# Kernel tuning notes

Hardware: AMD Instinct MI355X
Metric: run time of the kernel (lower is better)

## Reference

```python
import jax, jax.numpy as jnp
import numpy as np

N = 100000   # nodes
E = 3200000  # directed edges (avg degree 32)
T = 2048     # total flattened orders across all moves
M = 256      # number of moves (segments)


def _gat(x, src, dst, Wl, bl, Wr, br, att, b):
    # GATv2Conv (heads=1, eval mode -> attention dropout off), with self loops
    xl = x @ Wl.T + bl              # [N,10]
    xr = x @ Wr.T + br              # [N,10]
    sl = jnp.arange(N)
    s = jnp.concatenate([src, sl])
    d = jnp.concatenate([dst, sl])
    e = jax.nn.leaky_relu(xl[s] + xr[d], 0.2) @ att    # [E+N]
    emax = jax.ops.segment_max(e, d, num_segments=N)
    ex = jnp.exp(e - emax[d])
    den = jax.ops.segment_sum(ex, d, num_segments=N)
    return jax.ops.segment_sum((ex / den[d])[:, None] * xl[s], d, num_segments=N) + b


def setup_inputs() -> dict:
    key = jax.random.key(0)
    ks = iter(jax.random.split(key, 64))
    rn = lambda shape, s=0.1: jax.random.normal(next(ks), shape, jnp.float32) * s
    inp = {}
    inp['x1'] = rn((N, 15), 1.0)
    inp['x2'] = rn((1, 4), 1.0)
    src = jax.random.randint(next(ks), (E,), 0, N, jnp.int32)
    off = jax.random.randint(next(ks), (E,), 1, N, jnp.int32)
    inp['edge_src'] = src
    inp['edge_dst'] = ((src + off) % N).astype(jnp.int32)
    inp['move_type'] = jax.random.randint(next(ks), (T,), 0, 2, jnp.int32)
    inp['m_src'] = jax.random.randint(next(ks), (T,), 0, N, jnp.int32)
    inp['m_dst'] = jax.random.randint(next(ks), (T,), 0, N, jnp.int32)
    inp['m_target'] = jax.random.randint(next(ks), (T,), 0, N, jnp.int32)
    inp['m_armies'] = jax.random.uniform(next(ks), (T,), jnp.float32) * 10.0
    inp['move_id'] = (jnp.arange(T, dtype=jnp.int32) // (T // M))  # sorted, all segments non-empty
    # GATv2 layer params (in dims 15, 25, 25 -> out 10)
    for i, din in [(1, 15), (2, 25), (3, 25)]:
        inp[f'Wl{i}'] = rn((10, din)); inp[f'bl{i}'] = rn((10,))
        inp[f'Wr{i}'] = rn((10, din)); inp[f'br{i}'] = rn((10,))
        inp[f'att{i}'] = rn((10,));   inp[f'bias{i}'] = rn((10,))
    inp['lin_W'] = rn((15, 29)); inp['lin_b'] = rn((15,))
    inp['lin2_W'] = rn((1, 15)); inp['lin2_b'] = rn((1,))
    inp['aaa_W'] = rn((20, 48)); inp['aaa_b'] = rn((20,))
    inp['ccc_W'] = rn((20, 23)); inp['ccc_b'] = rn((20,))
    inp['attl_W'] = rn((1, 20)); inp['attl_b'] = rn((1,))
    inp['pi_W'] = rn((1, 20));   inp['pi_b'] = rn((1,))
    return inp


def reference(x1, x2, edge_src, edge_dst, move_type, m_src, m_dst, m_target, m_armies, move_id,
              Wl1, bl1, Wr1, br1, att1, bias1,
              Wl2, bl2, Wr2, br2, att2, bias2,
              Wl3, bl3, Wr3, br3, att3, bias3,
              lin_W, lin_b, lin2_W, lin2_b, aaa_W, aaa_b, ccc_W, ccc_b,
              attl_W, attl_b, pi_W, pi_b):
    h = jax.nn.relu(_gat(x1, edge_src, edge_dst, Wl1, bl1, Wr1, br1, att1, bias1))
    h = jax.nn.relu(_gat(jnp.concatenate([h, x1], 1), edge_src, edge_dst, Wl2, bl2, Wr2, br2, att2, bias2))
    x = jax.nn.relu(_gat(jnp.concatenate([h, x1], 1), edge_src, edge_dst, Wl3, bl3, Wr3, br3, att3, bias3))

    # per-order features (both branches computed, selected by move_type)
    extra = (0.6 * m_armies - 0.7 * (x1[m_dst, 3] + x1[m_dst, 4]))[:, None]
    feat_a = jnp.concatenate([x[m_src], x[m_dst], x1[m_src, 3:], x1[m_dst, 1:], m_armies[:, None], extra], axis=1)  # [T,48]
    a_out = jax.nn.relu(feat_a @ aaa_W.T + aaa_b)
    feat_d = jnp.concatenate([x[m_target], x1[m_target, 3:], m_armies[:, None]], axis=1)  # [T,23]
    d_out = jax.nn.relu(feat_d @ ccc_W.T + ccc_b)
    hm = jnp.where((move_type == 0)[:, None], a_out, d_out)  # [T,20]

    al = (hm @ attl_W.T + attl_b)[:, 0]   # [T]
    pi = (hm @ pi_W.T + pi_b)[:, 0]       # [T]
    amax = jax.ops.segment_max(al, move_id, num_segments=M)
    ex = jnp.exp(al - amax[move_id])
    den = jax.ops.segment_sum(ex, move_id, num_segments=M)
    p = jax.ops.segment_sum(ex / den[move_id] * pi, move_id, num_segments=M)  # [M]
    logp = jax.nn.log_softmax(p)

    x2t = jnp.tile(x2, (N, 1))
    v = jax.nn.relu(jnp.concatenate([x, x1, x2t], 1) @ lin_W.T + lin_b)
    V = jnp.tanh(jnp.mean(v @ lin2_W.T + lin2_b))
    return (V, logp)
```

## Files before the change

kernel.cpp:

```cpp
#include <hip/hip_runtime.h>
#include <cmath>

#define NN 100000
#define NE 3200000
#define TT 2048
#define MM 256
#define STR 16
#define HSTR 16
#define BSZ 64
#define NB 1563
#define EPB 16384
#define NBLK 196
#define SCAP 3072
#define PCAP 4096
#define CMAX 12
#define SRTP_CAP 5500000

__device__ __forceinline__ void atomicMaxF(float* addr, float v) {
    if (v >= 0.f) atomicMax((int*)addr, __float_as_int(v));
    else          atomicMin((unsigned int*)addr, __float_as_uint(v));
}

__device__ __forceinline__ unsigned short f2bf(float x) {
    unsigned u = __float_as_uint(x);
    u += 0x7FFFu + ((u >> 16) & 1u);
    return (unsigned short)(u >> 16);
}

__device__ __forceinline__ void unpack10(uint4 q, unsigned q2, float* a) {
    a[0] = __uint_as_float(q.x << 16);
    a[1] = __uint_as_float(q.x & 0xFFFF0000u);
    a[2] = __uint_as_float(q.y << 16);
    a[3] = __uint_as_float(q.y & 0xFFFF0000u);
    a[4] = __uint_as_float(q.z << 16);
    a[5] = __uint_as_float(q.z & 0xFFFF0000u);
    a[6] = __uint_as_float(q.w << 16);
    a[7] = __uint_as_float(q.w & 0xFFFF0000u);
    a[8] = __uint_as_float(q2 << 16);
    a[9] = __uint_as_float(q2 & 0xFFFF0000u);
}

__global__ __launch_bounds__(1024) void init_kernel(int* bcounts, int* pcounts, float* amax,
                                                    float* den_m, float* num_m, float* Vsum) {
    int i = blockIdx.x * 1024 + threadIdx.x;
    if (i < NB) { bcounts[i] = 0; pcounts[i] = 0; }
    if (i < MM) { amax[i] = -INFINITY; den_m[i] = 0.f; num_m[i] = 0.f; }
    if (i == 0) Vsum[0] = 0.f;
}

__global__ __launch_bounds__(256) void hist_kernel(const int* __restrict__ dst,
                                                   int* __restrict__ bcounts,
                                                   int* __restrict__ pcounts) {
    __shared__ int h[NB];
    int tid = threadIdx.x;
    for (int i = tid; i < NB; i += 256) h[i] = 0;
    __syncthreads();
    int base = blockIdx.x * EPB;
    int end = base + EPB; if (end > NE) end = NE;
    for (int i = base + tid * 4; i < end; i += 1024) {
        int4 d4 = *(const int4*)(dst + i);
        atomicAdd(&h[d4.x >> 6], 1);
        atomicAdd(&h[d4.y >> 6], 1);
        atomicAdd(&h[d4.z >> 6], 1);
        atomicAdd(&h[d4.w >> 6], 1);
    }
    __syncthreads();
    for (int i = tid; i < NB; i += 256) {
        int n = h[i];
        if (n) {
            atomicAdd(&bcounts[i], n);
            atomicAdd(&pcounts[i], (n + 15) & ~15);
        }
    }
}

__global__ __launch_bounds__(1024) void scan_kernel(const int* __restrict__ bcounts,
                                                    const int* __restrict__ pcounts,
                                                    int* __restrict__ bstart,
                                                    int* __restrict__ pbstart,
                                                    int* __restrict__ pcursor) {
    __shared__ int ssum[1024];
    __shared__ int psum[1024];
    int tid = threadIdx.x;
    const int per = (NB + 1023) / 1024;
    int base = tid * per;
    int s = 0, p = 0;
    for (int i = 0; i < per; i++) {
        int idx = base + i;
        if (idx < NB) { s += bcounts[idx]; p += pcounts[idx]; }
    }
    ssum[tid] = s; psum[tid] = p;
    __syncthreads();
    for (int off = 1; off < 1024; off <<= 1) {
        int v = (tid >= off) ? ssum[tid - off] : 0;
        int w = (tid >= off) ? psum[tid - off] : 0;
        __syncthreads();
        ssum[tid] += v; psum[tid] += w;
        __syncthreads();
    }
    int run = ssum[tid] - s;
    int prun = psum[tid] - p;
    for (int i = 0; i < per; i++) {
        int idx = base + i;
        if (idx < NB) {
            bstart[idx] = run;              run += bcounts[idx];
            pbstart[idx] = prun;
            pcursor[idx] = prun;            prun += pcounts[idx];
        }
    }
    if (tid == 0) { bstart[NB] = NE; pbstart[NB] = psum[1023]; }
}

__global__ __launch_bounds__(1024) void scatter_kernel(const int* __restrict__ src,
                                                       const int* __restrict__ dst,
                                                       int* __restrict__ pcursor,
                                                       int* __restrict__ srtp) {
    __shared__ int ent[EPB];
    __shared__ int cnt[NB];
    __shared__ int cur[NB];
    __shared__ int gbase[NB];
    __shared__ int psc[1024];
    int tid = threadIdx.x;
    for (int i = tid; i < NB; i += 1024) cnt[i] = 0;
    __syncthreads();
    int base = blockIdx.x * EPB;
    int end = base + EPB; if (end > NE) end = NE;
    for (int i = base + tid * 4; i < end; i += 4096) {
        int4 d4 = *(const int4*)(dst + i);
        atomicAdd(&cnt[d4.x >> 6], 1);
        atomicAdd(&cnt[d4.y >> 6], 1);
        atomicAdd(&cnt[d4.z >> 6], 1);
        atomicAdd(&cnt[d4.w >> 6], 1);
    }
    __syncthreads();
    const int PT = (NB + 1023) / 1024;
    int t0 = tid * PT;
    int s = 0;
    #pragma unroll
    for (int j = 0; j < PT; j++) { int idx = t0 + j; if (idx < NB) s += cnt[idx]; }
    psc[tid] = s;
    __syncthreads();
    for (int off = 1; off < 1024; off <<= 1) {
        int v = (tid >= off) ? psc[tid - off] : 0;
        __syncthreads();
        psc[tid] += v;
        __syncthreads();
    }
    int run = psc[tid] - s;
    #pragma unroll
    for (int j = 0; j < PT; j++) {
        int idx = t0 + j;
        if (idx < NB) { cur[idx] = run; run += cnt[idx]; }
    }
    for (int b = tid; b < NB; b += 1024) {
        int n = cnt[b];
        gbase[b] = n ? atomicAdd(&pcursor[b], (n + 15) & ~15) : 0;
    }
    __syncthreads();
    for (int i = base + tid * 4; i < end; i += 4096) {
        int4 d4 = *(const int4*)(dst + i);
        int4 s4 = *(const int4*)(src + i);
        int d, b, off;
        d = d4.x; b = d >> 6; off = atomicAdd(&cur[b], 1); ent[off] = ((d & 63) << 17) | s4.x;
        d = d4.y; b = d >> 6; off = atomicAdd(&cur[b], 1); ent[off] = ((d & 63) << 17) | s4.y;
        d = d4.z; b = d >> 6; off = atomicAdd(&cur[b], 1); ent[off] = ((d & 63) << 17) | s4.z;
        d = d4.w; b = d >> 6; off = atomicAdd(&cur[b], 1); ent[off] = ((d & 63) << 17) | s4.w;
    }
    __syncthreads();
    for (int b = tid; b < NB; b += 1024) {
        int n = cnt[b];
        if (!n) continue;
        int lb = cur[b] - n;
        int gb = gbase[b];
        int p16 = (n + 15) & ~15;
        for (int k = 0; k < p16; k += 4) {
            int4 v;
            v.x = (k + 0 < n) ? ent[lb + k + 0] : -1;
            v.y = (k + 1 < n) ? ent[lb + k + 1] : -1;
            v.z = (k + 2 < n) ? ent[lb + k + 2] : -1;
            v.w = (k + 3 < n) ? ent[lb + k + 3] : -1;
            *(int4*)(srtp + gb + k) = v;
        }
    }
}

__global__ __launch_bounds__(512) void sort2_kernel(const int* __restrict__ srtp,
                                                    const int* __restrict__ pbstart,
                                                    const int* __restrict__ bstart,
                                                    int* __restrict__ srt) {
    __shared__ int ent[PCAP];
    __shared__ int ent2[SCAP];
    __shared__ int cnts[BSZ];
    __shared__ int curs[BSZ];
    int b = blockIdx.x, tid = threadIdx.x;
    int p0 = pbstart[b], p1 = pbstart[b + 1];
    int pcnt = p1 - p0;
    if (pcnt > PCAP) pcnt = PCAP;
    if (tid < BSZ) cnts[tid] = 0;
    __syncthreads();
    for (int i = tid; i < pcnt; i += 512) {
        int p = srtp[p0 + i];
        ent[i] = p;
        if (p >= 0) atomicAdd(&cnts[p >> 17], 1);
    }
    __syncthreads();
    if (tid == 0) {
        int run = 0;
        for (int k = 0; k < BSZ; k++) { curs[k] = run; run += cnts[k]; }
    }
    __syncthreads();
    for (int i = tid; i < pcnt; i += 512) {
        int p = ent[i];
        if (p >= 0) {
            int pos = atomicAdd(&curs[p >> 17], 1);
            ent2[pos] = p;
        }
    }
    __syncthreads();
    int i0 = bstart[b];
    int cnt = bstart[b + 1] - i0;
    for (int i = tid; i < cnt; i += 512) srt[i0 + i] = ent2[i];
}

__global__ __launch_bounds__(256) void prep_kernel(
    const float* __restrict__ hprev,
    const float* __restrict__ x1,
    const float* __restrict__ Wl, const float* __restrict__ bl,
    const float* __restrict__ Wr, const float* __restrict__ br,
    unsigned short* __restrict__ xlh,
    unsigned short* __restrict__ xrh,
    int din)
{
    __shared__ float sWl[250], sWr[250], sbl[10], sbr[10];
    int tid = threadIdx.x;
    int nw = 10 * din;
    for (int i = tid; i < nw; i += blockDim.x) { sWl[i] = Wl[i]; sWr[i] = Wr[i]; }
    if (tid < 10) { sbl[tid] = bl[tid]; sbr[tid] = br[tid]; }
    __syncthreads();
    int n = blockIdx.x * blockDim.x + tid;
    if (n >= NN) return;

    float in[25];
    if (din == 15) {
        #pragma unroll
        for (int k = 0; k < 15; k++) in[k] = x1[n * 15 + k];
    } else {
        #pragma unroll
        for (int k = 0; k < 10; k++) in[k] = hprev[n * STR + k];
        #pragma unroll
        for (int k = 0; k < 15; k++) in[10 + k] = x1[n * 15 + k];
    }

    float slv[10], srv[10];
    #pragma unroll
    for (int j = 0; j < 10; j++) {
        float sl = sbl[j], sr = sbr[j];
        for (int k = 0; k < din; k++) {
            sl += in[k] * sWl[j * din + k];
            sr += in[k] * sWr[j * din + k];
        }
        slv[j] = sl; srv[j] = sr;
    }
    unsigned* lp = (unsigned*)(xlh + n * HSTR);
    unsigned* rp = (unsigned*)(xrh + n * HSTR);
    #pragma unroll
    for (int j = 0; j < 5; j++) {
        lp[j] = (unsigned)f2bf(slv[2 * j]) | ((unsigned)f2bf(slv[2 * j + 1]) << 16);
        rp[j] = (unsigned)f2bf(srv[2 * j]) | ((unsigned)f2bf(srv[2 * j + 1]) << 16);
    }
}

__global__ __launch_bounds__(256, 4) void gather_kernel(
    const int* __restrict__ srt, const int* __restrict__ bstart,
    const unsigned short* __restrict__ xlh, const unsigned short* __restrict__ xrh,
    const float* __restrict__ att, const float* __restrict__ bias,
    float* __restrict__ hout)
{
    __shared__ float accs[BSZ * 11];
    __shared__ float xrs[BSZ * 11];
    __shared__ float sat[10];
    int b = blockIdx.x, tid = threadIdx.x;
    if (tid < 10) sat[tid] = att[tid];
    __syncthreads();

    int n0 = b * BSZ;
    if (tid < BSZ) {
        int n = n0 + tid;
        if (n < NN) {
            const unsigned short* lr = xlh + n * HSTR;
            const unsigned short* rr = xrh + n * HSTR;
            uint4 ql = *(const uint4*)lr;  unsigned ql2 = *(const unsigned*)(lr + 8);
            uint4 qr = *(const uint4*)rr;  unsigned qr2 = *(const unsigned*)(rr + 8);
            float a[10], r[10];
            unpack10(ql, ql2, a);
            unpack10(qr, qr2, r);
            #pragma unroll
            for (int k = 0; k < 10; k++) xrs[tid * 11 + k] = r[k];
            float e = 0.f;
            #pragma unroll
            for (int k = 0; k < 10; k++) {
                float t = a[k] + r[k];
                t = t > 0.f ? t : 0.2f * t;
                e += sat[k] * t;
            }
            float ex = __expf(e);
            #pragma unroll
            for (int k = 0; k < 10; k++) accs[tid * 11 + k] = ex * a[k];
            accs[tid * 11 + 10] = ex;
        } else {
            #pragma unroll
            for (int k = 0; k < 11; k++) { accs[tid * 11 + k] = 0.f; xrs[tid * 11 + k] = 0.f; }
        }
    }
    __syncthreads();

    int i0 = bstart[b], i1 = bstart[b + 1];
    int cnt = i1 - i0;
    int C = (cnt + 255) >> 8;
    int a0 = i0 + tid * C;
    int a1 = a0 + C; if (a1 > i1) a1 = i1;
    int len = a1 - a0; if (len < 0) len = 0;
    if (len > 0) {
        int ps[CMAX];
        #pragma unroll
        for (int i = 0; i < CMAX; i++) ps[i] = (i < len) ? srt[a0 + i] : -1;

        const unsigned short* row0 = xlh + (ps[0] & 0x1FFFF) * HSTR;
        uint4 q = *(const uint4*)row0;
        unsigned q2 = *(const unsigned*)(row0 + 8);
        int cur = ps[0] >> 17;
        float racc[10];
        #pragma unroll
        for (int k = 0; k < 10; k++) racc[k] = 0.f;
        float rden = 0.f;
        #pragma unroll
        for (int i = 0; i < CMAX; i++) {
            if (i >= len) break;
            uint4 qn = q; unsigned q2n = q2;
            if (i + 1 < len) {
                const unsigned short* rn = xlh + (ps[i + 1] & 0x1FFFF) * HSTR;
                qn = *(const uint4*)rn;
                q2n = *(const unsigned*)(rn + 8);
            }
            int ld = ps[i] >> 17;
            if (ld != cur) {
                float* ac = accs + cur * 11;
                #pragma unroll
                for (int k = 0; k < 10; k++) atomicAdd(ac + k, racc[k]);
                atomicAdd(ac + 10, rden);
                #pragma unroll
                for (int k = 0; k < 10; k++) racc[k] = 0.f;
                rden = 0.f;
                cur = ld;
            }
            float a[10];
            unpack10(q, q2, a);
            const float* r = xrs + ld * 11;
            float e = 0.f;
            #pragma unroll
            for (int k = 0; k < 10; k++) {
                float t = a[k] + r[k];
                t = t > 0.f ? t : 0.2f * t;
                e += sat[k] * t;
            }
            float ex = __expf(e);
            rden += ex;
            #pragma unroll
            for (int k = 0; k < 10; k++) racc[k] += ex * a[k];
            q = qn; q2 = q2n;
        }
        float* ac = accs + cur * 11;
        #pragma unroll
        for (int k = 0; k < 10; k++) atomicAdd(ac + k, racc[k]);
        atomicAdd(ac + 10, rden);
    }
    __syncthreads();

    if (tid < BSZ) {
        int n = n0 + tid;
        if (n < NN) {
            float inv = 1.f / accs[tid * 11 + 10];
            #pragma unroll
            for (int k = 0; k < 10; k++) {
                float v = accs[tid * 11 + k] * inv + bias[k];
                hout[n * STR + k] = v > 0.f ? v : 0.f;
            }
        }
    }
}

__global__ __launch_bounds__(256) void value_kernel(
    const float* __restrict__ x, const float* __restrict__ x1, const float* __restrict__ x2,
    const float* __restrict__ lin_W, const float* __restrict__ lin_b,
    const float* __restrict__ lin2_W, const float* __restrict__ lin2_b,
    float* __restrict__ Vsum)
{
    __shared__ float sW[15 * 29], sb[15], sW2[15];
    __shared__ float red[256];
    int tid = threadIdx.x;
    for (int i = tid; i < 15 * 29; i += 256) sW[i] = lin_W[i];
    if (tid < 15) { sb[tid] = lin_b[tid]; sW2[tid] = lin2_W[tid]; }
    __syncthreads();
    int n = blockIdx.x * 256 + tid;
    float local = 0.f;
    if (n < NN) {
        float in[29];
        #pragma unroll
        for (int k = 0; k < 10; k++) in[k] = x[n * STR + k];
        #pragma unroll
        for (int k = 0; k < 15; k++) in[10 + k] = x1[n * 15 + k];
        #pragma unroll
        for (int k = 0; k < 4; k++) in[25 + k] = x2[k];
        float sc = lin2_b[0];
        #pragma unroll
        for (int j = 0; j < 15; j++) {
            float s = sb[j];
            for (int k = 0; k < 29; k++) s += in[k] * sW[j * 29 + k];
            sc += (s > 0.f ? s : 0.f) * sW2[j];
        }
        local = sc;
    }
    red[tid] = local;
    __syncthreads();
    for (int off = 128; off > 0; off >>= 1) {
        if (tid < off) red[tid] += red[tid + off];
        __syncthreads();
    }
    if (tid == 0) atomicAdd(Vsum, red[0]);
}

__global__ __launch_bounds__(256) void orders_kernel(
    const float* __restrict__ x, const float* __restrict__ x1,
    const int* __restrict__ move_type, const int* __restrict__ m_src,
    const int* __restrict__ m_dst, const int* __restrict__ m_target,
    const float* __restrict__ m_armies, const int* __restrict__ move_id,
    const float* __restrict__ aaa_W, const float* __restrict__ aaa_b,
    const float* __restrict__ ccc_W, const float* __restrict__ ccc_b,
    const float* __restrict__ attl_W, const float* __restrict__ attl_b,
    const float* __restrict__ pi_W, const float* __restrict__ pi_b,
    float* __restrict__ al_out, float* __restrict__ pi_out, float* __restrict__ amax)
{
    __shared__ float sA[20 * 48], sC[20 * 23], sAb[20], sCb[20];
    int tid = threadIdx.x;
    for (int i = tid; i < 20 * 48; i += 256) sA[i] = aaa_W[i];
    for (int i = tid; i < 20 * 23; i += 256) sC[i] = ccc_W[i];
    if (tid < 20) { sAb[tid] = aaa_b[tid]; sCb[tid] = ccc_b[tid]; }
    __syncthreads();
    int t = blockIdx.x * 256 + tid;
    if (t >= TT) return;

    float armies = m_armies[t];
    float hm[20];
    if (move_type[t] == 0) {
        int sn = m_src[t], dn = m_dst[t];
        float f[48];
        #pragma unroll
        for (int k = 0; k < 10; k++) f[k] = x[sn * STR + k];
        #pragma unroll
        for (int k = 0; k < 10; k++) f[10 + k] = x[dn * STR + k];
        #pragma unroll
        for (int k = 0; k < 12; k++) f[20 + k] = x1[sn * 15 + 3 + k];
        #pragma unroll
        for (int k = 0; k < 14; k++) f[32 + k] = x1[dn * 15 + 1 + k];
        f[46] = armies;
        f[47] = 0.6f * armies - 0.7f * (x1[dn * 15 + 3] + x1[dn * 15 + 4]);
        #pragma unroll
        for (int j = 0; j < 20; j++) {
            float s = sAb[j];
            for (int k = 0; k < 48; k++) s += f[k] * sA[j * 48 + k];
            hm[j] = s > 0.f ? s : 0.f;
        }
    } else {
        int tg = m_target[t];
        float f[23];
        #pragma unroll
        for (int k = 0; k < 10; k++) f[k] = x[tg * STR + k];
        #pragma unroll
        for (int k = 0; k < 12; k++) f[10 + k] = x1[tg * 15 + 3 + k];
        f[22] = armies;
        #pragma unroll
        for (int j = 0; j < 20; j++) {
            float s = sCb[j];
            for (int k = 0; k < 23; k++) s += f[k] * sC[j * 23 + k];
            hm[j] = s > 0.f ? s : 0.f;
        }
    }
    float a = attl_b[0], p = pi_b[0];
    #pragma unroll
    for (int j = 0; j < 20; j++) { a += hm[j] * attl_W[j]; p += hm[j] * pi_W[j]; }
    al_out[t] = a;
    pi_out[t] = p;
    atomicMaxF(&amax[move_id[t]], a);
}

__global__ __launch_bounds__(256) void orders2_kernel(
    const float* __restrict__ al, const float* __restrict__ piv,
    const int* __restrict__ move_id, const float* __restrict__ amax,
    float* __restrict__ den_m, float* __restrict__ num_m)
{
    int t = blockIdx.x * 256 + threadIdx.x;
    if (t >= TT) return;
    int m = move_id[t];
    float ex = __expf(al[t] - amax[m]);
    atomicAdd(den_m + m, ex);
    atomicAdd(num_m + m, ex * piv[t]);
}

__global__ __launch_bounds__(256) void final_kernel(
    const float* __restrict__ num_m, const float* __restrict__ den_m,
    const float* __restrict__ Vsum, float* __restrict__ out)
{
    __shared__ float sh[256];
    __shared__ float s_max, s_sum;
    int m = threadIdx.x;
    float p = num_m[m] / den_m[m];
    sh[m] = p;
    __syncthreads();
    for (int off = 128; off > 0; off >>= 1) {
        if (m < off) sh[m] = fmaxf(sh[m], sh[m + off]);
        __syncthreads();
    }
    if (m == 0) s_max = sh[0];
    __syncthreads();
    float e = __expf(p - s_max);
    sh[m] = e;
    __syncthreads();
    for (int off = 128; off > 0; off >>= 1) {
        if (m < off) sh[m] += sh[m + off];
        __syncthreads();
    }
    if (m == 0) s_sum = sh[0];
    __syncthreads();
    out[1 + m] = p - s_max - logf(s_sum);
    if (m == 0) out[0] = tanhf(Vsum[0] / (float)NN);
}

extern "C" void kernel_launch(void* const* d_in, const int* in_sizes, int n_in,
                              void* d_out, int out_size, void* d_ws, size_t ws_size,
                              hipStream_t stream) {
    const float* x1        = (const float*)d_in[0];
    const float* x2        = (const float*)d_in[1];
    const int*   esrc      = (const int*)d_in[2];
    const int*   edst      = (const int*)d_in[3];
    const int*   move_type = (const int*)d_in[4];
    const int*   m_src     = (const int*)d_in[5];
    const int*   m_dst     = (const int*)d_in[6];
    const int*   m_target  = (const int*)d_in[7];
    const float* m_armies  = (const float*)d_in[8];
    const int*   move_id   = (const int*)d_in[9];
    const float* W[3][6];
    for (int l = 0; l < 3; l++)
        for (int j = 0; j < 6; j++)
            W[l][j] = (const float*)d_in[10 + l * 6 + j];
    const float* lin_W  = (const float*)d_in[28];
    const float* lin_b  = (const float*)d_in[29];
    const float* lin2_W = (const float*)d_in[30];
    const float* lin2_b = (const float*)d_in[31];
    const float* aaa_W  = (const float*)d_in[32];
    const float* aaa_b  = (const float*)d_in[33];
    const float* ccc_W  = (const float*)d_in[34];
    const float* ccc_b  = (const float*)d_in[35];
    const float* attl_W = (const float*)d_in[36];
    const float* attl_b = (const float*)d_in[37];
    const float* pi_W   = (const float*)d_in[38];
    const float* pi_b   = (const float*)d_in[39];

    float* ws = (float*)d_ws;
    float* hA    = ws; ws += NN * STR;
    float* al    = ws; ws += TT;
    float* piv   = ws; ws += TT;
    float* amax  = ws; ws += MM;
    float* den_m = ws; ws += MM;
    float* num_m = ws; ws += MM;
    float* Vsum  = ws; ws += 1;
    unsigned short* xlh = (unsigned short*)ws; ws += NN * HSTR / 2;
    unsigned short* xrh = (unsigned short*)ws; ws += NN * HSTR / 2;
    int* iws = (int*)ws;
    int* bcounts = iws; iws += NB;
    int* pcounts = iws; iws += NB;
    int* bstart  = iws; iws += NB + 1;
    int* pbstart = iws; iws += NB + 1;
    int* pcursor = iws; iws += NB;
    int* srt     = iws; iws += NE;
    int* srtp    = iws; iws += SRTP_CAP;

    dim3 blk(256);
    dim3 gN((NN + 255) / 256);
    dim3 gT(TT / 256);

    init_kernel<<<dim3(2), dim3(1024), 0, stream>>>(bcounts, pcounts, amax, den_m, num_m, Vsum);
    hist_kernel<<<dim3(NBLK), blk, 0, stream>>>(edst, bcounts, pcounts);
    scan_kernel<<<dim3(1), dim3(1024), 0, stream>>>(bcounts, pcounts, bstart, pbstart, pcursor);
    scatter_kernel<<<dim3(NBLK), dim3(1024), 0, stream>>>(esrc, edst, pcursor, srtp);
    sort2_kernel<<<dim3(NB), dim3(512), 0, stream>>>(srtp, pbstart, bstart, srt);

    prep_kernel<<<gN, blk, 0, stream>>>(nullptr, x1, W[0][0], W[0][1], W[0][2], W[0][3], xlh, xrh, 15);
    gather_kernel<<<dim3(NB), blk, 0, stream>>>(srt, bstart, xlh, xrh, W[0][4], W[0][5], hA);

    prep_kernel<<<gN, blk, 0, stream>>>(hA, x1, W[1][0], W[1][1], W[1][2], W[1][3], xlh, xrh, 25);
    gather_kernel<<<dim3(NB), blk, 0, stream>>>(srt, bstart, xlh, xrh, W[1][4], W[1][5], hA);

    prep_kernel<<<gN, blk, 0, stream>>>(hA, x1, W[2][0], W[2][1], W[2][2], W[2][3], xlh, xrh, 25);
    gather_kernel<<<dim3(NB), blk, 0, stream>>>(srt, bstart, xlh, xrh, W[2][4], W[2][5], hA);

    value_kernel<<<gN, blk, 0, stream>>>(hA, x1, x2, lin_W, lin_b, lin2_W, lin2_b, Vsum);
    orders_kernel<<<gT, blk, 0, stream>>>(hA, x1, move_type, m_src, m_dst, m_target,
                                          m_armies, move_id, aaa_W, aaa_b, ccc_W, ccc_b,
                                          attl_W, attl_b, pi_W, pi_b, al, piv, amax);
    orders2_kernel<<<gT, blk, 0, stream>>>(al, piv, move_id, amax, den_m, num_m);
    final_kernel<<<dim3(1), blk, 0, stream>>>(num_m, den_m, Vsum, (float*)d_out);
}
```

Measured before the change: 437.8 us.

## Drop histogram/scan with fixed-capacity buckets and fuse GAT layers with next projection

Removes the histogram and prefix-scan passes by giving each destination bucket a fixed PCAP-sized slot. Bucket cursors are initialised inside the first projection kernel, and sort2 now sorts in place and records per-bucket counts. Each gather kernel now computes the next layer's bf16 projections, using double-buffered xl/xr arrays, and the last gather also computes the value head. The orders reduction is folded into the final kernel with shared-memory atomics. This cuts about eight launches and the intermediate hA round trips, at the cost of a larger padded workspace and silent truncation if any bucket exceeds PCAP.

```diff
diff --git a/kernel.cpp b/kernel.cpp
--- a/kernel.cpp
+++ b/kernel.cpp
@@ -14,7 +14,6 @@
 #define SCAP 3072
 #define PCAP 4096
 #define CMAX 12
-#define SRTP_CAP 5500000
 
 __device__ __forceinline__ void atomicMaxF(float* addr, float v) {
     if (v >= 0.f) atomicMax((int*)addr, __float_as_int(v));
@@ -40,75 +39,45 @@
     a[9] = __uint_as_float(q2 & 0xFFFF0000u);
 }
 
-__global__ __launch_bounds__(1024) void init_kernel(int* bcounts, int* pcounts, float* amax,
-                                                    float* den_m, float* num_m, float* Vsum) {
-    int i = blockIdx.x * 1024 + threadIdx.x;
-    if (i < NB) { bcounts[i] = 0; pcounts[i] = 0; }
-    if (i < MM) { amax[i] = -INFINITY; den_m[i] = 0.f; num_m[i] = 0.f; }
-    if (i == 0) Vsum[0] = 0.f;
-}
-
-__global__ __launch_bounds__(256) void hist_kernel(const int* __restrict__ dst,
-                                                   int* __restrict__ bcounts,
-                                                   int* __restrict__ pcounts) {
-    __shared__ int h[NB];
+__global__ __launch_bounds__(256) void init_prep1_kernel(
+    const float* __restrict__ x1,
+    const float* __restrict__ Wl, const float* __restrict__ bl,
+    const float* __restrict__ Wr, const float* __restrict__ br,
+    unsigned short* __restrict__ xlh, unsigned short* __restrict__ xrh,
+    int* __restrict__ pcursor, float* __restrict__ amax, float* __restrict__ Vsum)
+{
+    __shared__ float sWl[150], sWr[150], sbl[10], sbr[10];
     int tid = threadIdx.x;
-    for (int i = tid; i < NB; i += 256) h[i] = 0;
-    __syncthreads();
-    int base = blockIdx.x * EPB;
-    int end = base + EPB; if (end > NE) end = NE;
-    for (int i = base + tid * 4; i < end; i += 1024) {
-        int4 d4 = *(const int4*)(dst + i);
-        atomicAdd(&h[d4.x >> 6], 1);
-        atomicAdd(&h[d4.y >> 6], 1);
-        atomicAdd(&h[d4.z >> 6], 1);
-        atomicAdd(&h[d4.w >> 6], 1);
-    }
-    __syncthreads();
-    for (int i = tid; i < NB; i += 256) {
-        int n = h[i];
-        if (n) {
-            atomicAdd(&bcounts[i], n);
-            atomicAdd(&pcounts[i], (n + 15) & ~15);
-        }
-    }
-}
-
-__global__ __launch_bounds__(1024) void scan_kernel(const int* __restrict__ bcounts,
-                                                    const int* __restrict__ pcounts,
-                                                    int* __restrict__ bstart,
-                                                    int* __restrict__ pbstart,
-                                                    int* __restrict__ pcursor) {
-    __shared__ int ssum[1024];
-    __shared__ int psum[1024];
-    int tid = threadIdx.x;
-    const int per = (NB + 1023) / 1024;
-    int base = tid * per;
-    int s = 0, p = 0;
-    for (int i = 0; i < per; i++) {
-        int idx = base + i;
-        if (idx < NB) { s += bcounts[idx]; p += pcounts[idx]; }
-    }
-    ssum[tid] = s; psum[tid] = p;
-    __syncthreads();
-    for (int off = 1; off < 1024; off <<= 1) {
-        int v = (tid >= off) ? ssum[tid - off] : 0;
-        int w = (tid >= off) ? psum[tid - off] : 0;
-        __syncthreads();
-        ssum[tid] += v; psum[tid] += w;
-        __syncthreads();
-    }
-    int run = ssum[tid] - s;
-    int prun = psum[tid] - p;
-    for (int i = 0; i < per; i++) {
-        int idx = base + i;
-        if (idx < NB) {
-            bstart[idx] = run;              run += bcounts[idx];
-            pbstart[idx] = prun;
-            pcursor[idx] = prun;            prun += pcounts[idx];
-        }
-    }
-    if (tid == 0) { bstart[NB] = NE; pbstart[NB] = psum[1023]; }
+    for (int i = tid; i < 150; i += 256) { sWl[i] = Wl[i]; sWr[i] = Wr[i]; }
+    if (tid < 10) { sbl[tid] = bl[tid]; sbr[tid] = br[tid]; }
+    __syncthreads();
+    int gid = blockIdx.x * 256 + tid;
+    if (gid < NB) pcursor[gid] = gid * PCAP;
+    if (gid < MM) amax[gid] = -INFINITY;
+    if (gid == 0) Vsum[0] = 0.f;
+    int n = gid;
+    if (n >= NN) return;
+
+    float in[15];
+    #pragma unroll
+    for (int k = 0; k < 15; k++) in[k] = x1[n * 15 + k];
+
+    unsigned* lp = (unsigned*)(xlh + n * HSTR);
+    unsigned* rp = (unsigned*)(xrh + n * HSTR);
+    #pragma unroll
+    for (int jp = 0; jp < 5; jp++) {
+        float sl0 = sbl[2 * jp], sr0 = sbr[2 * jp];
+        float sl1 = sbl[2 * jp + 1], sr1 = sbr[2 * jp + 1];
+        for (int k = 0; k < 15; k++) {
+            float v = in[k];
+            sl0 += v * sWl[(2 * jp) * 15 + k];
+            sr0 += v * sWr[(2 * jp) * 15 + k];
+            sl1 += v * sWl[(2 * jp + 1) * 15 + k];
+            sr1 += v * sWr[(2 * jp + 1) * 15 + k];
+        }
+        lp[jp] = (unsigned)f2bf(sl0) | ((unsigned)f2bf(sl1) << 16);
+        rp[jp] = (unsigned)f2bf(sr0) | ((unsigned)f2bf(sr1) << 16);
+    }
 }
 
 __global__ __launch_bounds__(1024) void scatter_kernel(const int* __restrict__ src,
@@ -184,17 +153,16 @@
     }
 }
 
-__global__ __launch_bounds__(512) void sort2_kernel(const int* __restrict__ srtp,
-                                                    const int* __restrict__ pbstart,
-                                                    const int* __restrict__ bstart,
-                                                    int* __restrict__ srt) {
+__global__ __launch_bounds__(512) void sort2_kernel(int* __restrict__ srtp,
+                                                    const int* __restrict__ pcursor,
+                                                    int* __restrict__ bcounts) {
     __shared__ int ent[PCAP];
     __shared__ int ent2[SCAP];
     __shared__ int cnts[BSZ];
     __shared__ int curs[BSZ];
     int b = blockIdx.x, tid = threadIdx.x;
-    int p0 = pbstart[b], p1 = pbstart[b + 1];
-    int pcnt = p1 - p0;
+    int p0 = b * PCAP;
+    int pcnt = pcursor[b] - p0;
     if (pcnt > PCAP) pcnt = PCAP;
     if (tid < BSZ) cnts[tid] = 0;
     __syncthreads();
@@ -217,70 +185,27 @@
         }
     }
     __syncthreads();
-    int i0 = bstart[b];
-    int cnt = bstart[b + 1] - i0;
-    for (int i = tid; i < cnt; i += 512) srt[i0 + i] = ent2[i];
-}
-
-__global__ __launch_bounds__(256) void prep_kernel(
-    const float* __restrict__ hprev,
-    const float* __restrict__ x1,
-    const float* __restrict__ Wl, const float* __restrict__ bl,
-    const float* __restrict__ Wr, const float* __restrict__ br,
-    unsigned short* __restrict__ xlh,
-    unsigned short* __restrict__ xrh,
-    int din)
-{
-    __shared__ float sWl[250], sWr[250], sbl[10], sbr[10];
-    int tid = threadIdx.x;
-    int nw = 10 * din;
-    for (int i = tid; i < nw; i += blockDim.x) { sWl[i] = Wl[i]; sWr[i] = Wr[i]; }
-    if (tid < 10) { sbl[tid] = bl[tid]; sbr[tid] = br[tid]; }
-    __syncthreads();
-    int n = blockIdx.x * blockDim.x + tid;
-    if (n >= NN) return;
-
-    float in[25];
-    if (din == 15) {
-        #pragma unroll
-        for (int k = 0; k < 15; k++) in[k] = x1[n * 15 + k];
-    } else {
-        #pragma unroll
-        for (int k = 0; k < 10; k++) in[k] = hprev[n * STR + k];
-        #pragma unroll
-        for (int k = 0; k < 15; k++) in[10 + k] = x1[n * 15 + k];
-    }
-
-    float slv[10], srv[10];
-    #pragma unroll
-    for (int j = 0; j < 10; j++) {
-        float sl = sbl[j], sr = sbr[j];
-        for (int k = 0; k < din; k++) {
-            sl += in[k] * sWl[j * din + k];
-            sr += in[k] * sWr[j * din + k];
-        }
-        slv[j] = sl; srv[j] = sr;
-    }
-    unsigned* lp = (unsigned*)(xlh + n * HSTR);
-    unsigned* rp = (unsigned*)(xrh + n * HSTR);
-    #pragma unroll
-    for (int j = 0; j < 5; j++) {
-        lp[j] = (unsigned)f2bf(slv[2 * j]) | ((unsigned)f2bf(slv[2 * j + 1]) << 16);
-        rp[j] = (unsigned)f2bf(srv[2 * j]) | ((unsigned)f2bf(srv[2 * j + 1]) << 16);
-    }
-}
-
-__global__ __launch_bounds__(256, 4) void gather_kernel(
-    const int* __restrict__ srt, const int* __restrict__ bstart,
+    int cnt = curs[BSZ - 1];
+    for (int i = tid; i < cnt; i += 512) srtp[p0 + i] = ent2[i];
+    if (tid == 0) bcounts[b] = cnt;
+}
+
+__global__ __launch_bounds__(256, 4) void gather_mid_kernel(
+    const int* __restrict__ srtp, const int* __restrict__ bcounts,
     const unsigned short* __restrict__ xlh, const unsigned short* __restrict__ xrh,
     const float* __restrict__ att, const float* __restrict__ bias,
-    float* __restrict__ hout)
+    const float* __restrict__ x1,
+    const float* __restrict__ Wl2, const float* __restrict__ bl2,
+    const float* __restrict__ Wr2, const float* __restrict__ br2,
+    unsigned short* __restrict__ xlh_out, unsigned short* __restrict__ xrh_out)
 {
     __shared__ float accs[BSZ * 11];
     __shared__ float xrs[BSZ * 11];
     __shared__ float sat[10];
+    __shared__ float sWl2[250], sWr2[250], sbl2[10], sbr2[10];
     int b = blockIdx.x, tid = threadIdx.x;
-    if (tid < 10) sat[tid] = att[tid];
+    if (tid < 10) { sat[tid] = att[tid]; sbl2[tid] = bl2[tid]; sbr2[tid] = br2[tid]; }
+    for (int i = tid; i < 250; i += 256) { sWl2[i] = Wl2[i]; sWr2[i] = Wr2[i]; }
     __syncthreads();
 
     int n0 = b * BSZ;
@@ -314,16 +239,16 @@
     }
     __syncthreads();
 
-    int i0 = bstart[b], i1 = bstart[b + 1];
-    int cnt = i1 - i0;
+    int i0 = b * PCAP;
+    int cnt = bcounts[b];
     int C = (cnt + 255) >> 8;
     int a0 = i0 + tid * C;
-    int a1 = a0 + C; if (a1 > i1) a1 = i1;
+    int a1 = a0 + C; if (a1 > i0 + cnt) a1 = i0 + cnt;
     int len = a1 - a0; if (len < 0) len = 0;
     if (len > 0) {
         int ps[CMAX];
         #pragma unroll
-        for (int i = 0; i < CMAX; i++) ps[i] = (i < len) ? srt[a0 + i] : -1;
+        for (int i = 0; i < CMAX; i++) ps[i] = (i < len) ? srtp[a0 + i] : -1;
 
         const unsigned short* row0 = xlh + (ps[0] & 0x1FFFF) * HSTR;
         uint4 q = *(const uint4*)row0;
@@ -380,53 +305,181 @@
         int n = n0 + tid;
         if (n < NN) {
             float inv = 1.f / accs[tid * 11 + 10];
+            float in[25];
             #pragma unroll
             for (int k = 0; k < 10; k++) {
                 float v = accs[tid * 11 + k] * inv + bias[k];
-                hout[n * STR + k] = v > 0.f ? v : 0.f;
-            }
-        }
-    }
-}
-
-__global__ __launch_bounds__(256) void value_kernel(
-    const float* __restrict__ x, const float* __restrict__ x1, const float* __restrict__ x2,
+                in[k] = v > 0.f ? v : 0.f;
+            }
+            #pragma unroll
+            for (int k = 0; k < 15; k++) in[10 + k] = x1[n * 15 + k];
+            unsigned* lp = (unsigned*)(xlh_out + n * HSTR);
+            unsigned* rp = (unsigned*)(xrh_out + n * HSTR);
+            #pragma unroll
+            for (int jp = 0; jp < 5; jp++) {
+                float sl0 = sbl2[2 * jp], sr0 = sbr2[2 * jp];
+                float sl1 = sbl2[2 * jp + 1], sr1 = sbr2[2 * jp + 1];
+                for (int k = 0; k < 25; k++) {
+                    float v = in[k];
+                    sl0 += v * sWl2[(2 * jp) * 25 + k];
+                    sr0 += v * sWr2[(2 * jp) * 25 + k];
+                    sl1 += v * sWl2[(2 * jp + 1) * 25 + k];
+                    sr1 += v * sWr2[(2 * jp + 1) * 25 + k];
+                }
+                lp[jp] = (unsigned)f2bf(sl0) | ((unsigned)f2bf(sl1) << 16);
+                rp[jp] = (unsigned)f2bf(sr0) | ((unsigned)f2bf(sr1) << 16);
+            }
+        }
+    }
+}
+
+__global__ __launch_bounds__(256, 4) void gather_last_kernel(
+    const int* __restrict__ srtp, const int* __restrict__ bcounts,
+    const unsigned short* __restrict__ xlh, const unsigned short* __restrict__ xrh,
+    const float* __restrict__ att, const float* __restrict__ bias,
+    const float* __restrict__ x1, const float* __restrict__ x2,
     const float* __restrict__ lin_W, const float* __restrict__ lin_b,
     const float* __restrict__ lin2_W, const float* __restrict__ lin2_b,
-    float* __restrict__ Vsum)
+    float* __restrict__ hout, float* __restrict__ Vsum)
 {
-    __shared__ float sW[15 * 29], sb[15], sW2[15];
-    __shared__ float red[256];
-    int tid = threadIdx.x;
-    for (int i = tid; i < 15 * 29; i += 256) sW[i] = lin_W[i];
-    if (tid < 15) { sb[tid] = lin_b[tid]; sW2[tid] = lin2_W[tid]; }
-    __syncthreads();
-    int n = blockIdx.x * 256 + tid;
+    __shared__ float accs[BSZ * 11];
+    __shared__ float xrs[BSZ * 11];
+    __shared__ float sat[10];
+    __shared__ float sLW[15 * 29], sLb[15], sW2[15], sx2[4];
+    __shared__ float slin2b;
+    int b = blockIdx.x, tid = threadIdx.x;
+    if (tid < 10) sat[tid] = att[tid];
+    for (int i = tid; i < 15 * 29; i += 256) sLW[i] = lin_W[i];
+    if (tid < 15) { sLb[tid] = lin_b[tid]; sW2[tid] = lin2_W[tid]; }
+    if (tid < 4) sx2[tid] = x2[tid];
+    if (tid == 0) slin2b = lin2_b[0];
+    __syncthreads();
+
+    int n0 = b * BSZ;
+    if (tid < BSZ) {
+        int n = n0 + tid;
+        if (n < NN) {
+            const unsigned short* lr = xlh + n * HSTR;
+            const unsigned short* rr = xrh + n * HSTR;
+            uint4 ql = *(const uint4*)lr;  unsigned ql2 = *(const unsigned*)(lr + 8);
+            uint4 qr = *(const uint4*)rr;  unsigned qr2 = *(const unsigned*)(rr + 8);
+            float a[10], r[10];
+            unpack10(ql, ql2, a);
+            unpack10(qr, qr2, r);
+            #pragma unroll
+            for (int k = 0; k < 10; k++) xrs[tid * 11 + k] = r[k];
+            float e = 0.f;
+            #pragma unroll
+            for (int k = 0; k < 10; k++) {
+                float t = a[k] + r[k];
+                t = t > 0.f ? t : 0.2f * t;
+                e += sat[k] * t;
+            }
+            float ex = __expf(e);
+            #pragma unroll
+            for (int k = 0; k < 10; k++) accs[tid * 11 + k] = ex * a[k];
+            accs[tid * 11 + 10] = ex;
+        } else {
+            #pragma unroll
+            for (int k = 0; k < 11; k++) { accs[tid * 11 + k] = 0.f; xrs[tid * 11 + k] = 0.f; }
+        }
+    }
+    __syncthreads();
+
+    int i0 = b * PCAP;
+    int cnt = bcounts[b];
+    int C = (cnt + 255) >> 8;
+    int a0 = i0 + tid * C;
+    int a1 = a0 + C; if (a1 > i0 + cnt) a1 = i0 + cnt;
+    int len = a1 - a0; if (len < 0) len = 0;
+    if (len > 0) {
+        int ps[CMAX];
+        #pragma unroll
+        for (int i = 0; i < CMAX; i++) ps[i] = (i < len) ? srtp[a0 + i] : -1;
+
+        const unsigned short* row0 = xlh + (ps[0] & 0x1FFFF) * HSTR;
+        uint4 q = *(const uint4*)row0;
+        unsigned q2 = *(const unsigned*)(row0 + 8);
+        int cur = ps[0] >> 17;
+        float racc[10];
+        #pragma unroll
+        for (int k = 0; k < 10; k++) racc[k] = 0.f;
+        float rden = 0.f;
+        #pragma unroll
+        for (int i = 0; i < CMAX; i++) {
+            if (i >= len) break;
+            uint4 qn = q; unsigned q2n = q2;
+            if (i + 1 < len) {
+                const unsigned short* rn = xlh + (ps[i + 1] & 0x1FFFF) * HSTR;
+                qn = *(const uint4*)rn;
+                q2n = *(const unsigned*)(rn + 8);
+            }
+            int ld = ps[i] >> 17;
+            if (ld != cur) {
+                float* ac = accs + cur * 11;
+                #pragma unroll
+                for (int k = 0; k < 10; k++) atomicAdd(ac + k, racc[k]);
+                atomicAdd(ac + 10, rden);
+                #pragma unroll
+                for (int k = 0; k < 10; k++) racc[k] = 0.f;
+                rden = 0.f;
+                cur = ld;
+            }
+            float a[10];
+            unpack10(q, q2, a);
+            const float* r = xrs + ld * 11;
+            float e = 0.f;
+            #pragma unroll
+            for (int k = 0; k < 10; k++) {
+                float t = a[k] + r[k];
+                t = t > 0.f ? t : 0.2f * t;
+                e += sat[k] * t;
+            }
+            float ex = __expf(e);
+            rden += ex;
+            #pragma unroll
+            for (int k = 0; k < 10; k++) racc[k] += ex * a[k];
+            q = qn; q2 = q2n;
+        }
+        float* ac = accs + cur * 11;
+        #pragma unroll
+        for (int k = 0; k < 10; k++) atomicAdd(ac + k, racc[k]);
+        atomicAdd(ac + 10, rden);
+    }
+    __syncthreads();
+
     float local = 0.f;
-    if (n < NN) {
-        float in[29];
-        #pragma unroll
-        for (int k = 0; k < 10; k++) in[k] = x[n * STR + k];
-        #pragma unroll
-        for (int k = 0; k < 15; k++) in[10 + k] = x1[n * 15 + k];
-        #pragma unroll
-        for (int k = 0; k < 4; k++) in[25 + k] = x2[k];
-        float sc = lin2_b[0];
-        #pragma unroll
-        for (int j = 0; j < 15; j++) {
-            float s = sb[j];
-            for (int k = 0; k < 29; k++) s += in[k] * sW[j * 29 + k];
-            sc += (s > 0.f ? s : 0.f) * sW2[j];
-        }
-        local = sc;
-    }
-    red[tid] = local;
-    __syncthreads();
-    for (int off = 128; off > 0; off >>= 1) {
-        if (tid < off) red[tid] += red[tid + off];
-        __syncthreads();
-    }
-    if (tid == 0) atomicAdd(Vsum, red[0]);
+    if (tid < BSZ) {
+        int n = n0 + tid;
+        if (n < NN) {
+            float inv = 1.f / accs[tid * 11 + 10];
+            float in[29];
+            #pragma unroll
+            for (int k = 0; k < 10; k++) {
+                float v = accs[tid * 11 + k] * inv + bias[k];
+                v = v > 0.f ? v : 0.f;
+                hout[n * STR + k] = v;
+                in[k] = v;
+            }
+            #pragma unroll
+            for (int k = 0; k < 15; k++) in[10 + k] = x1[n * 15 + k];
+            #pragma unroll
+            for (int k = 0; k < 4; k++) in[25 + k] = sx2[k];
+            float sc = slin2b;
+            #pragma unroll
+            for (int j = 0; j < 15; j++) {
+                float s = sLb[j];
+                for (int k = 0; k < 29; k++) s += in[k] * sLW[j * 29 + k];
+                sc += (s > 0.f ? s : 0.f) * sW2[j];
+            }
+            local = sc;
+        }
+    }
+    if (tid < 64) {
+        #pragma unroll
+        for (int off = 32; off > 0; off >>= 1) local += __shfl_down(local, off, 64);
+        if (tid == 0) atomicAdd(Vsum, local);
+    }
 }
 
 __global__ __launch_bounds__(256) void orders_kernel(
@@ -493,27 +546,25 @@
     atomicMaxF(&amax[move_id[t]], a);
 }
 
-__global__ __launch_bounds__(256) void orders2_kernel(
+__global__ __launch_bounds__(256) void final2_kernel(
     const float* __restrict__ al, const float* __restrict__ piv,
     const int* __restrict__ move_id, const float* __restrict__ amax,
-    float* __restrict__ den_m, float* __restrict__ num_m)
-{
-    int t = blockIdx.x * 256 + threadIdx.x;
-    if (t >= TT) return;
-    int m = move_id[t];
-    float ex = __expf(al[t] - amax[m]);
-    atomicAdd(den_m + m, ex);
-    atomicAdd(num_m + m, ex * piv[t]);
-}
-
-__global__ __launch_bounds__(256) void final_kernel(
-    const float* __restrict__ num_m, const float* __restrict__ den_m,
     const float* __restrict__ Vsum, float* __restrict__ out)
 {
+    __shared__ float den_s[MM], num_s[MM];
     __shared__ float sh[256];
     __shared__ float s_max, s_sum;
     int m = threadIdx.x;
-    float p = num_m[m] / den_m[m];
+    den_s[m] = 0.f; num_s[m] = 0.f;
+    __syncthreads();
+    for (int t = m; t < TT; t += 256) {
+        int mid = move_id[t];
+        float ex = __expf(al[t] - amax[mid]);
+        atomicAdd(&den_s[mid], ex);
+        atomicAdd(&num_s[mid], ex * piv[t]);
+    }
+    __syncthreads();
+    float p = num_s[m] / den_s[m];
     sh[m] = p;
     __syncthreads();
     for (int off = 128; off > 0; off >>= 1) {
@@ -570,43 +621,40 @@
     float* al    = ws; ws += TT;
     float* piv   = ws; ws += TT;
     float* amax  = ws; ws += MM;
-    float* den_m = ws; ws += MM;
-    float* num_m = ws; ws += MM;
     float* Vsum  = ws; ws += 1;
-    unsigned short* xlh = (unsigned short*)ws; ws += NN * HSTR / 2;
-    unsigned short* xrh = (unsigned short*)ws; ws += NN * HSTR / 2;
+    unsigned short* xlhA = (unsigned short*)ws; ws += NN * HSTR / 2;
+    unsigned short* xrhA = (unsigned short*)ws; ws += NN * HSTR / 2;
+    unsigned short* xlhB = (unsigned short*)ws; ws += NN * HSTR / 2;
+    unsigned short* xrhB = (unsigned short*)ws; ws += NN * HSTR / 2;
     int* iws = (int*)ws;
+    int* pcursor = iws; iws += NB;
     int* bcounts = iws; iws += NB;
-    int* pcounts = iws; iws += NB;
-    int* bstart  = iws; iws += NB + 1;
-    int* pbstart = iws; iws += NB + 1;
-    int* pcursor = iws; iws += NB;
-    int* srt     = iws; iws += NE;
-    int* srtp    = iws; iws += SRTP_CAP;
+    int* srtp    = iws; iws += NB * PCAP;
 
     dim3 blk(256);
     dim3 gN((NN + 255) / 256);
     dim3 gT(TT / 256);
 
-    init_kernel<<<dim3(2), dim3(1024), 0, stream>>>(bcounts, pcounts, amax, den_m, num_m, Vsum);
-    hist_kernel<<<dim3(NBLK), blk, 0, stream>>>(edst, bcounts, pcounts);
-    scan_kernel<<<dim3(1), dim3(1024), 0, stream>>>(bcounts, pcounts, bstart, pbstart, pcursor);
+    init_prep1_kernel<<<gN, blk, 0, stream>>>(x1, W[0][0], W[0][1], W[0][2], W[0][3],
+                                              xlhA, xrhA, pcursor, amax, Vsum);
     scatter_kernel<<<dim3(NBLK), dim3(1024), 0, stream>>>(esrc, edst, pcursor, srtp);
-    sort2_kernel<<<dim3(NB), dim3(512), 0, stream>>>(srtp, pbstart, bstart, srt);
-
-    prep_kernel<<<gN, blk, 0, stream>>>(nullptr, x1, W[0][0], W[0][1], W[0][2], W[0][3], xlh, xrh, 15);
-    gather_kernel<<<dim3(NB), blk, 0, stream>>>(srt, bstart, xlh, xrh, W[0][4], W[0][5], hA);
-
-    prep_kernel<<<gN, blk, 0, stream>>>(hA, x1, W[1][0], W[1][1], W[1][2], W[1][3], xlh, xrh, 25);
-    gather_kernel<<<dim3(NB), blk, 0, stream>>>(srt, bstart, xlh, xrh, W[1][4], W[1][5], hA);
-
-    prep_kernel<<<gN, blk, 0, stream>>>(hA, x1, W[2][0], W[2][1], W[2][2], W[2][3], xlh, xrh, 25);
-    gather_kernel<<<dim3(NB), blk, 0, stream>>>(srt, bstart, xlh, xrh, W[2][4], W[2][5], hA);
-
-    value_kernel<<<gN, blk, 0, stream>>>(hA, x1, x2, lin_W, lin_b, lin2_W, lin2_b, Vsum);
+    sort2_kernel<<<dim3(NB), dim3(512), 0, stream>>>(srtp, pcursor, bcounts);
+
+    gather_mid_kernel<<<dim3(NB), blk, 0, stream>>>(srtp, bcounts, xlhA, xrhA,
+                                                    W[0][4], W[0][5], x1,
+                                                    W[1][0], W[1][1], W[1][2], W[1][3],
+                                                    xlhB, xrhB);
+    gather_mid_kernel<<<dim3(NB), blk, 0, stream>>>(srtp, bcounts, xlhB, xrhB,
+                                                    W[1][4], W[1][5], x1,
+                                                    W[2][0], W[2][1], W[2][2], W[2][3],
+                                                    xlhA, xrhA);
+    gather_last_kernel<<<dim3(NB), blk, 0, stream>>>(srtp, bcounts, xlhA, xrhA,
+                                                     W[2][4], W[2][5], x1, x2,
+                                                     lin_W, lin_b, lin2_W, lin2_b,
+                                                     hA, Vsum);
+
     orders_kernel<<<gT, blk, 0, stream>>>(hA, x1, move_type, m_src, m_dst, m_target,
                                           m_armies, move_id, aaa_W, aaa_b, ccc_W, ccc_b,
                                           attl_W, attl_b, pi_W, pi_b, al, piv, amax);
-    orders2_kernel<<<gT, blk, 0, stream>>>(al, piv, move_id, amax, den_m, num_m);
-    final_kernel<<<dim3(1), blk, 0, stream>>>(num_m, den_m, Vsum, (float*)d_out);
-}
+    final2_kernel<<<dim3(1), blk, 0, stream>>>(al, piv, move_id, amax, Vsum, (float*)d_out);
+}
```

New measurement: 411.6 us. 6.0% less time.
